# Optimization experiments

Measured on AMD Instinct MI355X. Metric: run time of the kernel, lower is better.

The kernel has to match this reference:

```python
import jax, jax.numpy as jnp
import numpy as np

B, S, IN, OUT = 16, 512, 512, 256
D, H, L, DFF = 1024, 16, 6, 2048
HD = D // H
SCALE = HD ** -0.5
HID = 256  # fc1/fc2 hidden size


def setup_inputs() -> dict:
    key = jax.random.key(0)
    ks = jax.random.split(key, 40)
    g = lambda i, shape, s=0.02: (jax.random.normal(ks[i], shape, jnp.float32) * s)
    z = lambda shape: jnp.zeros(shape, jnp.float32)
    o = lambda shape: jnp.ones(shape, jnp.float32)
    vec = jnp.zeros((B, S), jnp.int32).at[:, 0].set(1)  # one-hot rows (assert-only arg)
    return {
        "x": jax.random.normal(ks[0], (B, S, IN), jnp.float32),
        "xm": jax.random.uniform(ks[1], (B, S), jnp.float32),
        "vecSelector": vec,
        "proj_w": g(2, (IN, D)), "proj_b": z((D,)),
        "pos": g(3, (S, D)),
        "qw": g(4, (L, D, D)), "qb": z((L, D)),
        "kw": g(5, (L, D, D)), "kb": z((L, D)),
        "vw": g(6, (L, D, D)), "vb": z((L, D)),
        "ow": g(7, (L, D, D)), "ob": z((L, D)),
        "ln1_g": o((L, D)), "ln1_b": z((L, D)),
        "ln2_g": o((L, D)), "ln2_b": z((L, D)),
        "w1": g(8, (L, D, DFF)), "b1": z((L, DFF)),
        "w2": g(9, (L, DFF, D)), "b2": z((L, D)),
        "fc1_w": g(10, (D, HID)), "fc1_b": z((HID,)),
        "fc2_w": g(11, (HID, HID)), "fc2_b": z((HID,)),
        "fc3_w": g(12, (HID, OUT)), "fc3_b": z((OUT,)),
    }


def _ln(x, g, b, eps=1e-5):
    m = jnp.mean(x, -1, keepdims=True)
    v = jnp.mean((x - m) ** 2, -1, keepdims=True)
    return (x - m) * jax.lax.rsqrt(v + eps) * g + b


def reference(x, xm, vecSelector, proj_w, proj_b, pos, qw, qb, kw, kb, vw, vb,
              ow, ob, ln1_g, ln1_b, ln2_g, ln2_b, w1, b1, w2, b2,
              fc1_w, fc1_b, fc2_w, fc2_b, fc3_w, fc3_b):
    # linear_proj + positional encoding (pos[:, :d_model] == pos)
    h = x @ proj_w + proj_b + pos  # (B,S,D)
    # key padding mask: whole batch rows masked where xm.sum(-1)==0
    skpm = jnp.broadcast_to((jnp.sum(xm, -1) == 0)[:, None], (B, S))  # (B,S) bool
    neg_inf = jnp.float32(-jnp.inf)
    for i in range(L):
        q = (h @ qw[i] + qb[i]) * SCALE
        k = h @ kw[i] + kb[i]
        v = h @ vw[i] + vb[i]
        q = q.reshape(B, S, H, HD)
        k = k.reshape(B, S, H, HD)
        v = v.reshape(B, S, H, HD)
        sc = jnp.einsum('bthd,bshd->bhts', q, k)  # (B,H,T,S)
        sc = jnp.where(skpm[:, None, None, :], neg_inf, sc)
        # safe_softmax: clamp to [-10,10] THEN softmax (-inf -> -10)
        aw = jax.nn.softmax(jnp.clip(sc, -10.0, 10.0), axis=-1)
        ao = jnp.einsum('bhts,bshd->bthd', aw, v).reshape(B, S, D)
        ao = ao @ ow[i] + ob[i]
        # forward hook: clamp + softmax over embed dim
        ao = jax.nn.softmax(jnp.clip(ao, -10.0, 10.0), axis=-1)
        # torch _sa_block's `[0]` slices batch dim of the raw tensor -> (S,D),
        # broadcast-added to every batch row
        sa = ao[0]
        h = _ln(h + sa[None, :, :], ln1_g[i], ln1_b[i])
        ff = jax.nn.relu(h @ w1[i] + b1[i]) @ w2[i] + b2[i]
        h = _ln(h + ff, ln2_g[i], ln2_b[i])
    out = h @ fc1_w + fc1_b
    for _ in range(5):
        out = out @ fc2_w + fc2_b
    out = out @ fc3_w + fc3_b  # (B,S,OUT)
    return out
```

## Files before the change

### kernel.cpp

```cpp
#include <hip/hip_runtime.h>
#include <hip/hip_bf16.h>

using bf16 = __hip_bfloat16;
typedef __attribute__((ext_vector_type(8))) short short8v;
typedef __attribute__((ext_vector_type(4))) float floatx4;

constexpr int Bc = 16, Sc = 512, INc = 512, OUTc = 256;
constexpr int Dc = 1024, Hc = 16, Lc = 6, DFFc = 2048, HIDc = 256;
constexpr float SCALEc = 0.125f;
constexpr int QKVS = 3072;
constexpr size_t LSLOT = 8388608;

__device__ inline ushort f2b(float f) {
    union { float f; unsigned u; } v; v.f = f;
    unsigned r = (v.u + 0x7FFF + ((v.u >> 16) & 1)) >> 16;
    return (ushort)r;
}
__device__ inline float b2f(ushort b) {
    union { unsigned u; float f; } v; v.u = ((unsigned)b) << 16;
    return v.f;
}
__device__ inline float ldf(const float* p) { return *p; }
__device__ inline float ldf(const ushort* p) { return b2f(*p); }

__device__ inline void gll16(const ushort* g, ushort* l) {
    __builtin_amdgcn_global_load_lds(
        (const __attribute__((address_space(1))) unsigned int*)g,
        (__attribute__((address_space(3))) unsigned int*)l, 16, 0, 0);
}

__device__ inline float blockSum256(float v) {
    __shared__ float tmp[4];
#pragma unroll
    for (int o = 32; o > 0; o >>= 1) v += __shfl_xor(v, o, 64);
    int w = threadIdx.x >> 6;
    __syncthreads();
    if ((threadIdx.x & 63) == 0) tmp[w] = v;
    __syncthreads();
    return tmp[0] + tmp[1] + tmp[2] + tmp[3];
}
__device__ inline float blockMax256(float v) {
    __shared__ float tmp[4];
#pragma unroll
    for (int o = 32; o > 0; o >>= 1) v = fmaxf(v, __shfl_xor(v, o, 64));
    int w = threadIdx.x >> 6;
    __syncthreads();
    if ((threadIdx.x & 63) == 0) tmp[w] = v;
    __syncthreads();
    return fmaxf(fmaxf(tmp[0], tmp[1]), fmaxf(tmp[2], tmp[3]));
}

__global__ __launch_bounds__(256) void mask_k(const float* __restrict__ xm, float* __restrict__ flag) {
    float s = xm[threadIdx.x] + xm[threadIdx.x + 256];
    s = blockSum256(s);
    if (threadIdx.x == 0) flag[0] = (s == 0.f) ? 1.f : 0.f;
}

__global__ __launch_bounds__(256) void cvtx_k(const float* __restrict__ x, ushort* __restrict__ xb) {
    const size_t i = ((size_t)blockIdx.x * 256 + threadIdx.x) * 16;
    __align__(16) ushort o[16];
#pragma unroll
    for (int u = 0; u < 4; ++u) {
        float4 v = *(const float4*)&x[i + u * 4];
        o[u * 4 + 0] = f2b(v.x); o[u * 4 + 1] = f2b(v.y);
        o[u * 4 + 2] = f2b(v.z); o[u * 4 + 3] = f2b(v.w);
    }
    *(short8v*)&xb[i] = *(short8v*)&o[0];
    *(short8v*)&xb[i + 8] = *(short8v*)&o[8];
}

__global__ __launch_bounds__(256) void transp_k(const float* __restrict__ W, ushort* __restrict__ Wt,
                                                int K, int N, float wscale) {
    __shared__ float Ls[64][65];
    const int t = threadIdx.x;
    const int n0 = blockIdx.x * 64, k0 = blockIdx.y * 64;
    const int kr = t >> 4, n4 = (t & 15) * 4;
#pragma unroll
    for (int p = 0; p < 4; ++p) {
        float4 v = *(const float4*)&W[(size_t)(k0 + kr + p * 16) * N + n0 + n4];
        Ls[kr + p * 16][n4 + 0] = v.x; Ls[kr + p * 16][n4 + 1] = v.y;
        Ls[kr + p * 16][n4 + 2] = v.z; Ls[kr + p * 16][n4 + 3] = v.w;
    }
    __syncthreads();
    const int nr = t >> 4, k4 = (t & 15) * 4;
#pragma unroll
    for (int p = 0; p < 4; ++p) {
        ushort4 o;
        o.x = f2b(Ls[k4 + 0][nr + p * 16] * wscale); o.y = f2b(Ls[k4 + 1][nr + p * 16] * wscale);
        o.z = f2b(Ls[k4 + 2][nr + p * 16] * wscale); o.w = f2b(Ls[k4 + 3][nr + p * 16] * wscale);
        *(ushort4*)&Wt[(size_t)(n0 + nr + p * 16) * K + k0 + k4] = o;
    }
}

__global__ __launch_bounds__(256) void transpall_k(
    const float* __restrict__ qw, const float* __restrict__ kw, const float* __restrict__ vw,
    const float* __restrict__ ow, const float* __restrict__ w1, const float* __restrict__ w2,
    ushort* __restrict__ Wt, int l0, size_t lstride)
{
    const int l = l0 + blockIdx.y;
    ushort* slot = Wt + (size_t)blockIdx.y * lstride;
    const int id = blockIdx.x;
    int m, tx, ty;
    if (id < 1024)      { m = id >> 8; int r = id & 255;  tx = r & 15; ty = r >> 4; }
    else if (id < 1536) { m = 4;       int r = id - 1024; tx = r & 31; ty = r >> 5; }
    else                { m = 5;       int r = id - 1536; tx = r & 15; ty = r >> 4; }
    const float* W; ushort* dst; int K, N; float wscale = 1.f;
    switch (m) {
        case 0: W = qw + (size_t)l * Dc * Dc; K = Dc; N = Dc; dst = slot; wscale = SCALEc; break;
        case 1: W = kw + (size_t)l * Dc * Dc; K = Dc; N = Dc; dst = slot + 1048576; break;
        case 2: W = vw + (size_t)l * Dc * Dc; K = Dc; N = Dc; dst = slot + 2097152; break;
        case 3: W = ow + (size_t)l * Dc * Dc; K = Dc; N = Dc; dst = slot + 3145728; break;
        case 4: W = w1 + (size_t)l * Dc * DFFc; K = Dc; N = DFFc; dst = slot + 4194304; break;
        default: W = w2 + (size_t)l * DFFc * Dc; K = DFFc; N = Dc; dst = slot + 6291456; break;
    }
    __shared__ float Ls[64][65];
    const int t = threadIdx.x;
    const int n0 = tx * 64, k0 = ty * 64;
    const int kr = t >> 4, n4 = (t & 15) * 4;
#pragma unroll
    for (int p = 0; p < 4; ++p) {
        float4 v = *(const float4*)&W[(size_t)(k0 + kr + p * 16) * N + n0 + n4];
        Ls[kr + p * 16][n4 + 0] = v.x; Ls[kr + p * 16][n4 + 1] = v.y;
        Ls[kr + p * 16][n4 + 2] = v.z; Ls[kr + p * 16][n4 + 3] = v.w;
    }
    __syncthreads();
#pragma unroll
    for (int p = 0; p < 2; ++p) {
        const int idx = t + 256 * p;
        const int n = idx >> 3, kc = (idx & 7) * 8;
        __align__(16) ushort tmp[8];
#pragma unroll
        for (int u = 0; u < 8; ++u) tmp[u] = f2b(Ls[kc + u][n] * wscale);
        *(short8v*)&dst[(size_t)(n0 + n) * K + k0 + kc] = *(short8v*)tmp;
    }
}

template <int ACT, bool ADDPOS, int OMODE>
__global__ __launch_bounds__(256) void mgemm_k(
    const ushort* __restrict__ A, const ushort* __restrict__ Bt,
    const float* __restrict__ bias, const float* __restrict__ pos,
    float* __restrict__ Cf, ushort* __restrict__ Cb,
    int M, int N, int K, float scale)
{
    __shared__ __align__(16) ushort As[128 * 64];
    __shared__ __align__(16) ushort Bs[128 * 64];
    const int tid = threadIdx.x;
    const int nx = gridDim.x;
    const int nwg = nx * gridDim.y;
    int d = blockIdx.x + blockIdx.y * nx;
    if ((nwg & 7) == 0) d = (d & 7) * (nwg >> 3) + (d >> 3);
    const int m0 = (d / nx) * 128, n0 = (d % nx) * 128;
    const int lane = tid & 63, wv = tid >> 6;
    const int wm = (wv >> 1) * 64, wn = (wv & 1) * 64;
    floatx4 acc[4][4] = {};

    const int rA8 = lane >> 3, cch = lane & 7;

    for (int k0 = 0; k0 < K; k0 += 64) {
#pragma unroll
        for (int p = 0; p < 4; ++p) {
            const int r = wv * 32 + p * 8 + rA8;
            const int cs = (cch ^ (r & 7)) * 8;
            gll16(&Bt[(size_t)(n0 + r) * K + k0 + cs], &Bs[(wv * 32 + p * 8) * 64]);
            gll16(&A[(size_t)(m0 + r) * K + k0 + cs], &As[(wv * 32 + p * 8) * 64]);
        }
        __syncthreads();
#pragma unroll
        for (int s = 0; s < 2; ++s) {
            short8v af[4], bf_[4];
            const int kg = s * 32 + (lane >> 4) * 8;
#pragma unroll
            for (int f = 0; f < 4; ++f) {
                const int ra = wm + f * 16 + (lane & 15);
                af[f] = *(const short8v*)&As[ra * 64 + (kg ^ ((ra & 7) * 8))];
                const int rb = wn + f * 16 + (lane & 15);
                bf_[f] = *(const short8v*)&Bs[rb * 64 + (kg ^ ((rb & 7) * 8))];
            }
#pragma unroll
            for (int i = 0; i < 4; ++i)
#pragma unroll
                for (int j = 0; j < 4; ++j)
                    acc[i][j] = __builtin_amdgcn_mfma_f32_16x16x32_bf16(af[i], bf_[j], acc[i][j], 0, 0, 0);
        }
        __syncthreads();
    }

    const int cc = lane & 15, rr4 = (lane >> 4) * 4;
#pragma unroll
    for (int i = 0; i < 4; ++i) {
#pragma unroll
        for (int j = 0; j < 4; ++j) {
            const int col = n0 + wn + j * 16 + cc;
            const float bsv = bias[col];
#pragma unroll
            for (int q = 0; q < 4; ++q) {
                const int row = m0 + wm + i * 16 + rr4 + q;
                float v = acc[i][j][q] + bsv;
                if (ADDPOS) v += pos[(size_t)(row & (Sc - 1)) * N + col];
                v *= scale;
                if (ACT == 1) v = fmaxf(v, 0.f);
                if (OMODE == 0) Cf[(size_t)row * N + col] = v;
                else if (OMODE == 1) Cb[(size_t)row * N + col] = f2b(v);
                else { Cf[(size_t)row * N + col] = v; Cb[(size_t)row * N + col] = f2b(v); }
            }
        }
    }
}

template <int OMODE>
__global__ __launch_bounds__(256) void mgemm64_k(
    const ushort* __restrict__ A, const ushort* __restrict__ Bt,
    const float* __restrict__ bias,
    float* __restrict__ Cf, ushort* __restrict__ Cb,
    int M, int N, int K)
{
    __shared__ __align__(16) ushort As[64 * 64];
    __shared__ __align__(16) ushort Bs[64 * 64];
    const int tid = threadIdx.x;
    const int nx = gridDim.x;
    const int nwg = nx * gridDim.y;
    int d = blockIdx.x + blockIdx.y * nx;
    if ((nwg & 7) == 0) d = (d & 7) * (nwg >> 3) + (d >> 3);
    const int m0 = (d / nx) * 64, n0 = (d % nx) * 64;
    const int lane = tid & 63, wv = tid >> 6;
    floatx4 acc[4] = {};

    const int rA8 = lane >> 3, cch = lane & 7;

    for (int k0 = 0; k0 < K; k0 += 64) {
#pragma unroll
        for (int p = 0; p < 2; ++p) {
            const int r = wv * 16 + p * 8 + rA8;
            const int cs = (cch ^ (r & 7)) * 8;
            gll16(&A[(size_t)(m0 + r) * K + k0 + cs], &As[(wv * 16 + p * 8) * 64]);
            gll16(&Bt[(size_t)(n0 + r) * K + k0 + cs], &Bs[(wv * 16 + p * 8) * 64]);
        }
        __syncthreads();
#pragma unroll
        for (int s = 0; s < 2; ++s) {
            const int kg = s * 32 + (lane >> 4) * 8;
            const int rb = wv * 16 + (lane & 15);
            short8v bf_ = *(const short8v*)&Bs[rb * 64 + (kg ^ ((rb & 7) * 8))];
#pragma unroll
            for (int f = 0; f < 4; ++f) {
                const int ra = f * 16 + (lane & 15);
                short8v af = *(const short8v*)&As[ra * 64 + (kg ^ ((ra & 7) * 8))];
                acc[f] = __builtin_amdgcn_mfma_f32_16x16x32_bf16(af, bf_, acc[f], 0, 0, 0);
            }
        }
        __syncthreads();
    }

    const int cc = lane & 15, rr4 = (lane >> 4) * 4;
    const int col = n0 + wv * 16 + cc;
    const float bsv = bias[col];
#pragma unroll
    for (int f = 0; f < 4; ++f) {
#pragma unroll
        for (int q = 0; q < 4; ++q) {
            const int row = m0 + f * 16 + rr4 + q;
            float v = acc[f][q] + bsv;
            if (OMODE == 0) Cf[(size_t)row * N + col] = v;
            else            Cb[(size_t)row * N + col] = f2b(v);
        }
    }
}

#define SG256(ts, g) do { \
    if ((ts) < NT) { \
        const int sb_ = (ts) & 1; \
        const int kk_ = (ts) << 6; \
        _Pragma("unroll") \
        for (int ii_ = 0; ii_ < 2; ++ii_) { \
            const int ib_ = wv * 16 + ii_ * 8; \
            if ((g) == 0 || (g) == 2) { \
                const int r0_ = (ib_ < 64 ? ib_ : ib_ + 64) + (((g) == 2) ? 64 : 0); \
                const int rr_ = r0_ + rA8; \
                gll16(A + (size_t)(m0 + rr_) * K + kk_ + ((cch ^ (rr_ & 7)) << 3), \
                      &Al[sb_][r0_ * 64]); \
            } else { \
                const int r0_ = ((ib_ >> 5) * 64) + (ib_ & 31) + (((g) == 3) ? 32 : 0); \
                const int rr_ = r0_ + rA8; \
                gll16(Bt + (size_t)(n0 + rr_) * K + kk_ + ((cch ^ (rr_ & 7)) << 3), \
                      &Bl[sb_][r0_ * 64]); \
            } \
        } \
    } } while (0)

#define LDA256(bb, fb) \
    _Pragma("unroll") for (int f_ = 0; f_ < 4; ++f_) { \
        const int ra_ = wm + ((fb) + f_) * 16 + (lane & 15); \
        const int sw_ = (ra_ & 7) * 8; \
        af[f_][0] = *(const short8v*)&Al[bb][ra_ * 64 + ((kgl) ^ sw_)]; \
        af[f_][1] = *(const short8v*)&Al[bb][ra_ * 64 + ((32 + kgl) ^ sw_)]; }

#define LDB256(bb, jb) \
    _Pragma("unroll") for (int f_ = 0; f_ < 2; ++f_) { \
        const int rb_ = wn + ((jb) + f_) * 16 + (lane & 15); \
        const int sw_ = (rb_ & 7) * 8; \
        bf_[(jb) + f_][0] = *(const short8v*)&Bl[bb][rb_ * 64 + ((kgl) ^ sw_)]; \
        bf_[(jb) + f_][1] = *(const short8v*)&Bl[bb][rb_ * 64 + ((32 + kgl) ^ sw_)]; }

#define MM256(ib, jb) \
    __builtin_amdgcn_s_setprio(1); \
    _Pragma("unroll") for (int i_ = 0; i_ < 4; ++i_) \
    _Pragma("unroll") for (int j_ = 0; j_ < 2; ++j_) \
    _Pragma("unroll") for (int s_ = 0; s_ < 2; ++s_) \
        acc[(ib) + i_][(jb) + j_] = __builtin_amdgcn_mfma_f32_16x16x32_bf16( \
            af[i_][s_], bf_[(jb) + j_][s_], acc[(ib) + i_][(jb) + j_], 0, 0, 0); \
    __builtin_amdgcn_s_setprio(0);

__global__ __launch_bounds__(512) void mgemm256_k(
    const ushort* __restrict__ A, const ushort* __restrict__ Bt,
    const float* __restrict__ bias, ushort* __restrict__ Cb,
    int M, int N, int K, int ACT)
{
    __shared__ __align__(16) ushort Al[2][256 * 64];
    __shared__ __align__(16) ushort Bl[2][256 * 64];
    const int tid = threadIdx.x;
    const int lane = tid & 63, wv = tid >> 6;
    const int nx = gridDim.x, nwg = nx * gridDim.y;
    int d = blockIdx.x + blockIdx.y * nx;
    if ((nwg & 7) == 0) d = (d & 7) * (nwg >> 3) + (d >> 3);
    const int m0 = (d / nx) * 256, n0 = (d % nx) * 256;
    const int wm = (wv >> 2) * 128, wn = (wv & 3) * 64;
    const int rA8 = lane >> 3, cch = lane & 7;
    const int kgl = (lane >> 4) * 8;
    const int NT = K >> 6;
    floatx4 acc[8][4] = {};
    short8v af[4][2], bf_[4][2];

    SG256(0, 0); SG256(0, 1); SG256(0, 2); SG256(0, 3);
    SG256(1, 0); SG256(1, 1); SG256(1, 2);
    asm volatile("s_waitcnt vmcnt(6)" ::: "memory");
    __builtin_amdgcn_s_barrier();

    for (int t = 0; t < NT; ++t) {
        const int bb = t & 1;
        if (t + 1 < NT) { asm volatile("s_waitcnt vmcnt(6)" ::: "memory"); }
        else            { asm volatile("s_waitcnt vmcnt(0)" ::: "memory"); }
        LDA256(bb, 0); LDB256(bb, 0);
        SG256(t + 1, 3);
        __builtin_amdgcn_s_barrier();
        MM256(0, 0);
        __builtin_amdgcn_s_barrier();
        LDB256(bb, 2);
        SG256(t + 2, 0);
        __builtin_amdgcn_s_barrier();
        MM256(0, 2);
        __builtin_amdgcn_s_barrier();
        LDA256(bb, 4);
        SG256(t + 2, 1);
        __builtin_amdgcn_s_barrier();
        MM256(4, 0);
        __builtin_amdgcn_s_barrier();
        SG256(t + 2, 2);
        __builtin_amdgcn_s_barrier();
        MM256(4, 2);
        __builtin_amdgcn_s_barrier();
    }

    const int cc = lane & 15, rr4 = (lane >> 4) * 4;
#pragma unroll
    for (int i = 0; i < 8; ++i) {
#pragma unroll
        for (int j = 0; j < 4; ++j) {
            const int col = n0 + wn + j * 16 + cc;
            const float bsv = bias[col];
#pragma unroll
            for (int q = 0; q < 4; ++q) {
                const int row = m0 + wm + i * 16 + rr4 + q;
                float v = acc[i][j][q] + bsv;
                if (ACT) v = fmaxf(v, 0.f);
                Cb[(size_t)row * N + col] = f2b(v);
            }
        }
    }
}

__global__ __launch_bounds__(256) void fattn_k(
    const ushort* __restrict__ qkv, ushort* __restrict__ ao, const float* __restrict__ flag)
{
    const int hh = blockIdx.y;
    const int t0 = blockIdx.x * 16;
    __shared__ __align__(16) ushort Qs[16 * 64];
    __shared__ __align__(16) ushort Ks[64 * 64];
    __shared__ float Vs[64][68];
    __shared__ float Ps[16][68];
    __shared__ float rs[4][16];
    const int tid = threadIdx.x;
    const int lane = tid & 63, wv = tid >> 6;
    const bool msk = flag[0] > 0.5f;

    if (tid < 128) {
        const int r = tid >> 3, c = tid & 7;
        short8v q = *(const short8v*)&qkv[(size_t)(t0 + r) * QKVS + hh * 64 + c * 8];
        *(short8v*)&Qs[r * 64 + ((c * 8) ^ ((r & 7) * 8))] = q;
    }
    if (tid < 64) ((float*)rs)[tid] = 0.f;

    float o[4] = {};
    const int pq = tid >> 4, pd = (tid & 15) * 4;

    for (int s0 = 0; s0 < Sc; s0 += 64) {
        __syncthreads();
        {
            const int vr = tid >> 2, vc = (tid & 3) * 16;
            const ushort* vsrc = &qkv[(size_t)(s0 + vr) * QKVS + 2048 + hh * 64 + vc];
            short8v v0 = *(const short8v*)vsrc, v1 = *(const short8v*)(vsrc + 8);
#pragma unroll
            for (int u = 0; u < 8; ++u) {
                Vs[vr][vc + u] = b2f((ushort)v0[u]);
                Vs[vr][vc + 8 + u] = b2f((ushort)v1[u]);
            }
#pragma unroll
            for (int u = 0; u < 2; ++u) {
                const int task = tid + u * 256;
                const int kr = task >> 3, kc = task & 7;
                short8v kvv = *(const short8v*)&qkv[(size_t)(s0 + kr) * QKVS + 1024 + hh * 64 + kc * 8];
                *(short8v*)&Ks[kr * 64 + ((kc * 8) ^ ((kr & 7) * 8))] = kvv;
            }
        }
        __syncthreads();
        floatx4 pacc = {};
#pragma unroll
        for (int s = 0; s < 2; ++s) {
            const int kg = s * 32 + (lane >> 4) * 8;
            const int ra = lane & 15;
            short8v aq = *(const short8v*)&Qs[ra * 64 + (kg ^ ((ra & 7) * 8))];
            const int rb = 16 * wv + (lane & 15);
            short8v bk = *(const short8v*)&Ks[rb * 64 + (kg ^ ((rb & 7) * 8))];
            pacc = __builtin_amdgcn_mfma_f32_16x16x32_bf16(aq, bk, pacc, 0, 0, 0);
        }
        const int cc = lane & 15, rr4 = (lane >> 4) * 4;
#pragma unroll
        for (int q = 0; q < 4; ++q) {
            float v = fminf(fmaxf(pacc[q], -10.f), 10.f);
            if (msk) v = -10.f;
            float e = __expf(v - 10.f);
            Ps[rr4 + q][wv * 16 + cc] = e;
            float rsum = e;
            rsum += __shfl_xor(rsum, 1, 64);
            rsum += __shfl_xor(rsum, 2, 64);
            rsum += __shfl_xor(rsum, 4, 64);
            rsum += __shfl_xor(rsum, 8, 64);
            if (cc == 0) rs[wv][rr4 + q] += rsum;
        }
        __syncthreads();
#pragma unroll 8
        for (int ss = 0; ss < 64; ++ss) {
            float p = Ps[pq][ss];
#pragma unroll
            for (int u = 0; u < 4; ++u) o[u] += p * Vs[ss][pd + u];
        }
    }
    __syncthreads();
    float inv = 1.f / (rs[0][pq] + rs[1][pq] + rs[2][pq] + rs[3][pq]);
#pragma unroll
    for (int u = 0; u < 4; ++u)
        ao[(size_t)(t0 + pq) * Dc + hh * 64 + pd + u] = f2b(o[u] * inv);
}

template <int ACT, bool OUT_BF16, bool HASB>
__global__ __launch_bounds__(256) void gemm_k(
    const float* __restrict__ A, const float* __restrict__ W,
    const float* __restrict__ bias,
    float* __restrict__ Cf, bf16* __restrict__ Cb,
    int M, int N, int K, float scale)
{
    __shared__ float As[16][68];
    __shared__ float Ws[16][68];
    const int tid = threadIdx.x;
    const int m0 = blockIdx.y * 64, n0 = blockIdx.x * 64;
    const int ty = tid >> 4, tx = tid & 15;
    float c[4][4] = {};

    const int ka = tid & 15, mb = tid >> 4;
    const int nw = tid & 63, kb = tid >> 6;

    for (int k0 = 0; k0 < K; k0 += 16) {
#pragma unroll
        for (int j = 0; j < 4; ++j) {
            int m = mb + 16 * j;
            As[ka][m] = A[(size_t)(m0 + m) * K + k0 + ka];
        }
#pragma unroll
        for (int j = 0; j < 4; ++j) {
            int k = kb + 4 * j;
            Ws[k][nw] = W[(size_t)(k0 + k) * N + n0 + nw];
        }
        __syncthreads();
#pragma unroll
        for (int k = 0; k < 16; ++k) {
            float4 av = *(const float4*)&As[k][ty * 4];
            float4 wv = *(const float4*)&Ws[k][tx * 4];
            float a[4] = {av.x, av.y, av.z, av.w};
            float w[4] = {wv.x, wv.y, wv.z, wv.w};
#pragma unroll
            for (int i = 0; i < 4; ++i)
#pragma unroll
                for (int j = 0; j < 4; ++j) c[i][j] += a[i] * w[j];
        }
        __syncthreads();
    }

#pragma unroll
    for (int i = 0; i < 4; ++i) {
        int m = m0 + ty * 4 + i;
#pragma unroll
        for (int j = 0; j < 4; ++j) {
            int n = n0 + tx * 4 + j;
            float v = c[i][j] + (HASB ? bias[n] : 0.f);
            v *= scale;
            if (ACT == 1) v = fmaxf(v, 0.f);
            if (OUT_BF16) Cb[(size_t)m * N + n] = __float2bfloat16(v);
            else          Cf[(size_t)m * N + n] = v;
        }
    }
}

__global__ __launch_bounds__(256) void biaschain_k(
    const float* __restrict__ fc1b, const float* __restrict__ fc2w, const float* __restrict__ fc2b,
    const float* __restrict__ fc3w, const float* __restrict__ fc3b, float* __restrict__ bc)
{
    __shared__ float vs[256];
    const int t = threadIdx.x;
    float v = fc1b[t];
    for (int r = 0; r < 5; ++r) {
        vs[t] = v; __syncthreads();
        float s = fc2b[t];
#pragma unroll 8
        for (int k = 0; k < 256; ++k) s += vs[k] * fc2w[k * 256 + t];
        v = s; __syncthreads();
    }
    vs[t] = v; __syncthreads();
    float s = fc3b[t];
#pragma unroll 8
    for (int k = 0; k < 256; ++k) s += vs[k] * fc3w[k * 256 + t];
    bc[t] = s;
}

__global__ __launch_bounds__(256) void qkvbiasall_k(
    const float* __restrict__ qb, const float* __restrict__ kb, const float* __restrict__ vb,
    float* __restrict__ o)
{
    int i = blockIdx.x * 256 + threadIdx.x;
    int l = i / QKVS, j = i - l * QKVS;
    float v = (j < 1024) ? qb[l * Dc + j] * SCALEc
            : (j < 2048) ? kb[l * Dc + j - 1024] : vb[l * Dc + j - 2048];
    o[i] = v;
}

__global__ __launch_bounds__(256) void smaddln_k(
    ushort* __restrict__ hb, const float* __restrict__ obv,
    const float* __restrict__ g, const float* __restrict__ b)
{
    const int row = blockIdx.x;
    const float* op = obv + (size_t)(row & (Sc - 1)) * Dc;
    ushort* hp = hb + (size_t)row * Dc;
    const int c0 = threadIdx.x * 4;
    float4 ov = *(const float4*)&op[c0];
    float r[4] = {ov.x, ov.y, ov.z, ov.w};
    float mx = -1e30f;
#pragma unroll
    for (int j = 0; j < 4; ++j) { r[j] = fminf(fmaxf(r[j], -10.f), 10.f); mx = fmaxf(mx, r[j]); }
    mx = blockMax256(mx);
    float s = 0.f;
#pragma unroll
    for (int j = 0; j < 4; ++j) { r[j] = __expf(r[j] - mx); s += r[j]; }
    s = blockSum256(s);
    float sinv = 1.f / s;
    ushort4 hv = *(const ushort4*)&hp[c0];
    float x[4] = {b2f(hv.x), b2f(hv.y), b2f(hv.z), b2f(hv.w)};
    float ssum = 0.f;
#pragma unroll
    for (int j = 0; j < 4; ++j) { x[j] += r[j] * sinv; ssum += x[j]; }
    float mean = blockSum256(ssum) * (1.f / (float)Dc);
    float vsum = 0.f;
#pragma unroll
    for (int j = 0; j < 4; ++j) { float d_ = x[j] - mean; vsum += d_ * d_; }
    float var = blockSum256(vsum) * (1.f / (float)Dc);
    float inv = rsqrtf(var + 1e-5f);
    float4 gv = *(const float4*)&g[c0];
    float4 bv = *(const float4*)&b[c0];
    ushort4 o4;
    o4.x = f2b((x[0] - mean) * inv * gv.x + bv.x);
    o4.y = f2b((x[1] - mean) * inv * gv.y + bv.y);
    o4.z = f2b((x[2] - mean) * inv * gv.z + bv.z);
    o4.w = f2b((x[3] - mean) * inv * gv.w + bv.w);
    *(ushort4*)&hp[c0] = o4;
}

__global__ __launch_bounds__(256) void add_ln_k(
    ushort* __restrict__ hb, const ushort* __restrict__ add,
    const float* __restrict__ g, const float* __restrict__ b)
{
    const int row = blockIdx.x;
    const ushort* ap = add + (size_t)row * Dc;
    ushort* hp = hb + (size_t)row * Dc;
    const int c0 = threadIdx.x * 4;
    ushort4 hv = *(const ushort4*)&hp[c0];
    float x[4] = {b2f(hv.x), b2f(hv.y), b2f(hv.z), b2f(hv.w)};
#pragma unroll
    for (int j = 0; j < 4; ++j) x[j] += ldf(&ap[c0 + j]);
    float s = x[0] + x[1] + x[2] + x[3];
    float mean = blockSum256(s) * (1.f / (float)Dc);
    float vsum = 0.f;
#pragma unroll
    for (int j = 0; j < 4; ++j) { float d = x[j] - mean; vsum += d * d; }
    float var = blockSum256(vsum) * (1.f / (float)Dc);
    float inv = rsqrtf(var + 1e-5f);
    float4 gv = *(const float4*)&g[c0];
    float4 bv = *(const float4*)&b[c0];
    ushort4 ov;
    ov.x = f2b((x[0] - mean) * inv * gv.x + bv.x);
    ov.y = f2b((x[1] - mean) * inv * gv.y + bv.y);
    ov.z = f2b((x[2] - mean) * inv * gv.z + bv.z);
    ov.w = f2b((x[3] - mean) * inv * gv.w + bv.w);
    *(ushort4*)&hp[c0] = ov;
}

extern "C" void kernel_launch(void* const* d_in, const int* in_sizes, int n_in,
                              void* d_out, int out_size, void* d_ws, size_t ws_size,
                              hipStream_t stream)
{
    const float* x      = (const float*)d_in[0];
    const float* xm     = (const float*)d_in[1];
    const float* proj_w = (const float*)d_in[3];
    const float* proj_b = (const float*)d_in[4];
    const float* pos    = (const float*)d_in[5];
    const float* qw     = (const float*)d_in[6];
    const float* qb     = (const float*)d_in[7];
    const float* kw     = (const float*)d_in[8];
    const float* kb     = (const float*)d_in[9];
    const float* vw     = (const float*)d_in[10];
    const float* vb     = (const float*)d_in[11];
    const float* ow     = (const float*)d_in[12];
    const float* obias  = (const float*)d_in[13];
    const float* ln1g   = (const float*)d_in[14];
    const float* ln1b   = (const float*)d_in[15];
    const float* ln2g   = (const float*)d_in[16];
    const float* ln2b   = (const float*)d_in[17];
    const float* w1     = (const float*)d_in[18];
    const float* b1     = (const float*)d_in[19];
    const float* w2     = (const float*)d_in[20];
    const float* b2     = (const float*)d_in[21];
    const float* fc1w   = (const float*)d_in[22];
    const float* fc1b   = (const float*)d_in[23];
    const float* fc2w   = (const float*)d_in[24];
    const float* fc2b   = (const float*)d_in[25];
    const float* fc3w   = (const float*)d_in[26];
    const float* fc3b   = (const float*)d_in[27];

    float* ws = (float*)d_ws;
    const size_t HSZ = (size_t)Bc * Sc * Dc;
    ushort* hb  = (ushort*)ws;
    ushort* ffu = (ushort*)(ws + HSZ / 2);
    float*  rgA = ws + HSZ;
    float*  meta = ws + 2 * HSZ;
    float*  flag = meta;
    float*  qkvball = meta + 256;
    ushort* Wt = (ushort*)(ws + 2 * HSZ + 262144);

    const bool big = ws_size >= (size_t)163 * 1024 * 1024;
    const size_t lstride = big ? LSLOT : 0;
    ushort* projWt = big ? Wt + (size_t)6 * LSLOT : Wt;

    ushort* qkvfu = (ushort*)rgA;
    ushort* aovu  = (ushort*)(rgA + 786432);
    float*  obv   = rgA + 1048576;
    ushort* midu  = (ushort*)rgA;
    ushort* xb    = (ushort*)rgA;
    float* W2  = rgA;
    float* W4  = rgA + 65536;
    float* W5  = rgA + 131072;
    float* C1  = rgA + 196608;
    float* Wc  = rgA + 458752;
    float* bcv = rgA + 720896;

    const int MR = Bc * Sc;

    mask_k<<<1, 256, 0, stream>>>(xm, flag);
    qkvbiasall_k<<<72, 256, 0, stream>>>(qb, kb, vb, qkvball);
    if (big)
        transpall_k<<<dim3(2048, 6), 256, 0, stream>>>(qw, kw, vw, ow, w1, w2, Wt, 0, lstride);

    cvtx_k<<<(MR * INc) / (256 * 16), 256, 0, stream>>>(x, xb);
    transp_k<<<dim3(Dc / 64, INc / 64), 256, 0, stream>>>(proj_w, projWt, INc, Dc, 1.f);
    mgemm_k<0, true, 1><<<dim3(Dc / 128, MR / 128), 256, 0, stream>>>(
        xb, projWt, proj_b, pos, nullptr, hb, MR, Dc, INc, 1.f);

    for (int l = 0; l < Lc; ++l) {
        ushort* slot = Wt + (size_t)(big ? l : 0) * LSLOT;
        const float* ob_l = obias + l * Dc;
        const float* b1_l = b1 + l * DFFc;
        const float* b2_l = b2 + l * Dc;

        if (!big)
            transpall_k<<<dim3(2048, 1), 256, 0, stream>>>(qw, kw, vw, ow, w1, w2, Wt, l, 0);

        mgemm64_k<1><<<dim3(QKVS / 64, Sc / 64), 256, 0, stream>>>(
            hb, slot, qkvball + l * QKVS, nullptr, qkvfu, Sc, QKVS, Dc);
        fattn_k<<<dim3(Sc / 16, Hc), 256, 0, stream>>>(qkvfu, aovu, flag);
        mgemm64_k<0><<<dim3(Dc / 64, Sc / 64), 256, 0, stream>>>(
            aovu, slot + 3145728, ob_l, obv, nullptr, Sc, Dc, Dc);
        smaddln_k<<<MR, 256, 0, stream>>>(hb, obv, ln1g + l * Dc, ln1b + l * Dc);

        mgemm256_k<<<dim3(DFFc / 256, MR / 256), 512, 0, stream>>>(
            hb, slot + 4194304, b1_l, midu, MR, DFFc, Dc, 1);
        mgemm_k<0, false, 1><<<dim3(Dc / 128, MR / 128), 256, 0, stream>>>(
            midu, slot + 6291456, b2_l, nullptr, nullptr, ffu, MR, Dc, DFFc, 1.f);
        add_ln_k<<<MR, 256, 0, stream>>>(hb, ffu, ln2g + l * Dc, ln2b + l * Dc);
    }

    gemm_k<0, false, false><<<dim3(4, 4), 256, 0, stream>>>(
        fc2w, fc2w, nullptr, W2, nullptr, HIDc, HIDc, HIDc, 1.f);
    gemm_k<0, false, false><<<dim3(4, 4), 256, 0, stream>>>(
        W2, W2, nullptr, W4, nullptr, HIDc, HIDc, HIDc, 1.f);
    gemm_k<0, false, false><<<dim3(4, 4), 256, 0, stream>>>(
        W4, fc2w, nullptr, W5, nullptr, HIDc, HIDc, HIDc, 1.f);
    gemm_k<0, false, false><<<dim3(4, 16), 256, 0, stream>>>(
        fc1w, W5, nullptr, C1, nullptr, Dc, HIDc, HIDc, 1.f);
    gemm_k<0, false, false><<<dim3(4, 16), 256, 0, stream>>>(
        C1, fc3w, nullptr, Wc, nullptr, Dc, HIDc, HIDc, 1.f);
    biaschain_k<<<1, 256, 0, stream>>>(fc1b, fc2w, fc2b, fc3w, fc3b, bcv);
    transp_k<<<dim3(HIDc / 64, Dc / 64), 256, 0, stream>>>(Wc, Wt, Dc, HIDc, 1.f);
    mgemm64_k<0><<<dim3(HIDc / 64, MR / 64), 256, 0, stream>>>(
        hb, Wt, bcv, (float*)d_out, nullptr, MR, HIDc, Dc);
}
```

Before: 1.215 ms.

## Add 256x128 pipelined MFMA GEMM for w2 and projection; enlarge transpose tiles

Adds a new 512-thread GEMM kernel with 256x128 tiles, double-buffered LDS and direct global-to-LDS loads. It replaces the 128x128 kernel for the FFN w2 GEMM and the input projection, aiming for more operand reuse per workgroup and better overlap of loads with MFMA work. The 256x256 kernel's vmcnt wait is moved to the end of each iteration so loads stay in flight across the MFMA phases. The weight transpose kernel now handles 256x64 tiles per block, launching a quarter as many blocks, at the cost of a larger LDS footprint.

```diff
diff --git a/kernel.cpp b/kernel.cpp
--- a/kernel.cpp
+++ b/kernel.cpp
@@ -101,9 +101,9 @@
     ushort* slot = Wt + (size_t)blockIdx.y * lstride;
     const int id = blockIdx.x;
     int m, tx, ty;
-    if (id < 1024)      { m = id >> 8; int r = id & 255;  tx = r & 15; ty = r >> 4; }
-    else if (id < 1536) { m = 4;       int r = id - 1024; tx = r & 31; ty = r >> 5; }
-    else                { m = 5;       int r = id - 1536; tx = r & 15; ty = r >> 4; }
+    if (id < 256)      { m = id >> 6; int r = id & 63;  tx = r & 15; ty = r >> 4; }
+    else if (id < 384) { m = 4;       int r = id - 256; tx = r & 31; ty = r >> 5; }
+    else               { m = 5;       int r = id - 384; tx = r & 15; ty = r >> 4; }
     const float* W; ushort* dst; int K, N; float wscale = 1.f;
     switch (m) {
         case 0: W = qw + (size_t)l * Dc * Dc; K = Dc; N = Dc; dst = slot; wscale = SCALEc; break;
@@ -113,21 +113,22 @@
         case 4: W = w1 + (size_t)l * Dc * DFFc; K = Dc; N = DFFc; dst = slot + 4194304; break;
         default: W = w2 + (size_t)l * DFFc * Dc; K = DFFc; N = Dc; dst = slot + 6291456; break;
     }
-    __shared__ float Ls[64][65];
+    __shared__ float Ls[256][65];
     const int t = threadIdx.x;
-    const int n0 = tx * 64, k0 = ty * 64;
-    const int kr = t >> 4, n4 = (t & 15) * 4;
-#pragma unroll
-    for (int p = 0; p < 4; ++p) {
-        float4 v = *(const float4*)&W[(size_t)(k0 + kr + p * 16) * N + n0 + n4];
-        Ls[kr + p * 16][n4 + 0] = v.x; Ls[kr + p * 16][n4 + 1] = v.y;
-        Ls[kr + p * 16][n4 + 2] = v.z; Ls[kr + p * 16][n4 + 3] = v.w;
+    const int n0 = tx * 64, k0 = ty * 256;
+    const int krb = t >> 4, n4 = (t & 15) * 4;
+#pragma unroll
+    for (int p = 0; p < 16; ++p) {
+        const int r = krb + p * 16;
+        float4 v = *(const float4*)&W[(size_t)(k0 + r) * N + n0 + n4];
+        Ls[r][n4 + 0] = v.x; Ls[r][n4 + 1] = v.y;
+        Ls[r][n4 + 2] = v.z; Ls[r][n4 + 3] = v.w;
     }
     __syncthreads();
 #pragma unroll
-    for (int p = 0; p < 2; ++p) {
+    for (int p = 0; p < 8; ++p) {
         const int idx = t + 256 * p;
-        const int n = idx >> 3, kc = (idx & 7) * 8;
+        const int n = idx >> 5, kc = (idx & 31) * 8;
         __align__(16) ushort tmp[8];
 #pragma unroll
         for (int u = 0; u < 8; ++u) tmp[u] = f2b(Ls[kc + u][n] * wscale);
@@ -337,8 +338,6 @@
 
     for (int t = 0; t < NT; ++t) {
         const int bb = t & 1;
-        if (t + 1 < NT) { asm volatile("s_waitcnt vmcnt(6)" ::: "memory"); }
-        else            { asm volatile("s_waitcnt vmcnt(0)" ::: "memory"); }
         LDA256(bb, 0); LDB256(bb, 0);
         SG256(t + 1, 3);
         __builtin_amdgcn_s_barrier();
@@ -357,6 +356,8 @@
         SG256(t + 2, 2);
         __builtin_amdgcn_s_barrier();
         MM256(4, 2);
+        if (t + 2 < NT) { asm volatile("s_waitcnt vmcnt(6)" ::: "memory"); }
+        else            { asm volatile("s_waitcnt vmcnt(0)" ::: "memory"); }
         __builtin_amdgcn_s_barrier();
     }
 
@@ -376,6 +377,126 @@
             }
         }
     }
+}
+
+__global__ __launch_bounds__(512) void mgemm256x128_k(
+    const ushort* __restrict__ A, const ushort* __restrict__ Bt,
+    const float* __restrict__ bias, const float* __restrict__ pos, int addpos,
+    float* __restrict__ Cf, ushort* __restrict__ Cb, int omode,
+    int M, int N, int K, int ACT)
+{
+    __shared__ __align__(16) ushort Al[2][256 * 64];
+    __shared__ __align__(16) ushort Bl[2][128 * 64];
+    const int tid = threadIdx.x;
+    const int lane = tid & 63, wv = tid >> 6;
+    const int nx = gridDim.x, nwg = nx * gridDim.y;
+    int d = blockIdx.x + blockIdx.y * nx;
+    if ((nwg & 7) == 0) d = (d & 7) * (nwg >> 3) + (d >> 3);
+    const int m0 = (d / nx) * 256, n0 = (d % nx) * 128;
+    const int wm = (wv >> 1) * 64, wn = (wv & 1) * 64;
+    const int rA8 = lane >> 3, cch = lane & 7;
+    const int kgl = (lane >> 4) * 8;
+    const int NT = K >> 6;
+    floatx4 acc[4][4] = {};
+    short8v af[2][2], bf_[4][2];
+
+#define SGA(ts, g) do { \
+    if ((ts) < NT) { \
+        const int sb_ = (ts) & 1; \
+        const int kk_ = (ts) << 6; \
+        _Pragma("unroll") \
+        for (int ii_ = 0; ii_ < 2; ++ii_) { \
+            const int r0_ = (wv >> 1) * 64 + ((g) ? 32 : 0) + (wv & 1) * 16 + ii_ * 8; \
+            const int rr_ = r0_ + rA8; \
+            gll16(A + (size_t)(m0 + rr_) * K + kk_ + ((cch ^ (rr_ & 7)) << 3), \
+                  &Al[sb_][r0_ * 64]); \
+        } \
+    } } while (0)
+#define SGB(ts) do { \
+    if ((ts) < NT) { \
+        const int sb_ = (ts) & 1; \
+        const int kk_ = (ts) << 6; \
+        _Pragma("unroll") \
+        for (int ii_ = 0; ii_ < 2; ++ii_) { \
+            const int r0_ = wv * 16 + ii_ * 8; \
+            const int rr_ = r0_ + rA8; \
+            gll16(Bt + (size_t)(n0 + rr_) * K + kk_ + ((cch ^ (rr_ & 7)) << 3), \
+                  &Bl[sb_][r0_ * 64]); \
+        } \
+    } } while (0)
+#define LDAX(bb, fb) \
+    _Pragma("unroll") for (int f_ = 0; f_ < 2; ++f_) { \
+        const int ra_ = wm + ((fb) + f_) * 16 + (lane & 15); \
+        const int sw_ = (ra_ & 7) * 8; \
+        af[f_][0] = *(const short8v*)&Al[bb][ra_ * 64 + ((kgl) ^ sw_)]; \
+        af[f_][1] = *(const short8v*)&Al[bb][ra_ * 64 + ((32 + kgl) ^ sw_)]; }
+#define LDBX(bb, jb) \
+    _Pragma("unroll") for (int f_ = 0; f_ < 2; ++f_) { \
+        const int rb_ = wn + ((jb) + f_) * 16 + (lane & 15); \
+        const int sw_ = (rb_ & 7) * 8; \
+        bf_[(jb) + f_][0] = *(const short8v*)&Bl[bb][rb_ * 64 + ((kgl) ^ sw_)]; \
+        bf_[(jb) + f_][1] = *(const short8v*)&Bl[bb][rb_ * 64 + ((32 + kgl) ^ sw_)]; }
+#define MMX(ia, jb) \
+    __builtin_amdgcn_s_setprio(1); \
+    _Pragma("unroll") for (int i_ = 0; i_ < 2; ++i_) \
+    _Pragma("unroll") for (int j_ = 0; j_ < 2; ++j_) \
+    _Pragma("unroll") for (int s_ = 0; s_ < 2; ++s_) \
+        acc[(ia) + i_][(jb) + j_] = __builtin_amdgcn_mfma_f32_16x16x32_bf16( \
+            af[i_][s_], bf_[(jb) + j_][s_], acc[(ia) + i_][(jb) + j_], 0, 0, 0); \
+    __builtin_amdgcn_s_setprio(0);
+
+    SGA(0, 0); SGA(0, 1); SGB(0);
+    SGA(1, 0); SGA(1, 1);
+    asm volatile("s_waitcnt vmcnt(4)" ::: "memory");
+    __builtin_amdgcn_s_barrier();
+
+    for (int t = 0; t < NT; ++t) {
+        const int bb = t & 1;
+        LDAX(bb, 0); LDBX(bb, 0);
+        SGB(t + 1);
+        __builtin_amdgcn_s_barrier();
+        MMX(0, 0);
+        __builtin_amdgcn_s_barrier();
+        LDBX(bb, 2);
+        SGA(t + 2, 0);
+        __builtin_amdgcn_s_barrier();
+        MMX(0, 2);
+        __builtin_amdgcn_s_barrier();
+        LDAX(bb, 2);
+        __builtin_amdgcn_s_barrier();
+        MMX(2, 0);
+        __builtin_amdgcn_s_barrier();
+        SGA(t + 2, 1);
+        __builtin_amdgcn_s_barrier();
+        MMX(2, 2);
+        if (t + 2 < NT) { asm volatile("s_waitcnt vmcnt(4)" ::: "memory"); }
+        else            { asm volatile("s_waitcnt vmcnt(0)" ::: "memory"); }
+        __builtin_amdgcn_s_barrier();
+    }
+
+    const int cc = lane & 15, rr4 = (lane >> 4) * 4;
+#pragma unroll
+    for (int i = 0; i < 4; ++i) {
+#pragma unroll
+        for (int j = 0; j < 4; ++j) {
+            const int col = n0 + wn + j * 16 + cc;
+            const float bsv = bias[col];
+#pragma unroll
+            for (int q = 0; q < 4; ++q) {
+                const int row = m0 + wm + i * 16 + rr4 + q;
+                float v = acc[i][j][q] + bsv;
+                if (addpos) v += pos[(size_t)(row & (Sc - 1)) * N + col];
+                if (ACT) v = fmaxf(v, 0.f);
+                if (omode == 0) Cf[(size_t)row * N + col] = v;
+                else            Cb[(size_t)row * N + col] = f2b(v);
+            }
+        }
+    }
+#undef SGA
+#undef SGB
+#undef LDAX
+#undef LDBX
+#undef MMX
 }
 
 __global__ __launch_bounds__(256) void fattn_k(
@@ -683,12 +804,12 @@
     mask_k<<<1, 256, 0, stream>>>(xm, flag);
     qkvbiasall_k<<<72, 256, 0, stream>>>(qb, kb, vb, qkvball);
     if (big)
-        transpall_k<<<dim3(2048, 6), 256, 0, stream>>>(qw, kw, vw, ow, w1, w2, Wt, 0, lstride);
+        transpall_k<<<dim3(512, 6), 256, 0, stream>>>(qw, kw, vw, ow, w1, w2, Wt, 0, lstride);
 
     cvtx_k<<<(MR * INc) / (256 * 16), 256, 0, stream>>>(x, xb);
     transp_k<<<dim3(Dc / 64, INc / 64), 256, 0, stream>>>(proj_w, projWt, INc, Dc, 1.f);
-    mgemm_k<0, true, 1><<<dim3(Dc / 128, MR / 128), 256, 0, stream>>>(
-        xb, projWt, proj_b, pos, nullptr, hb, MR, Dc, INc, 1.f);
+    mgemm256x128_k<<<dim3(Dc / 128, MR / 256), 512, 0, stream>>>(
+        xb, projWt, proj_b, pos, 1, nullptr, hb, 1, MR, Dc, INc, 0);
 
     for (int l = 0; l < Lc; ++l) {
         ushort* slot = Wt + (size_t)(big ? l : 0) * LSLOT;
@@ -697,7 +818,7 @@
         const float* b2_l = b2 + l * Dc;
 
         if (!big)
-            transpall_k<<<dim3(2048, 1), 256, 0, stream>>>(qw, kw, vw, ow, w1, w2, Wt, l, 0);
+            transpall_k<<<dim3(512, 1), 256, 0, stream>>>(qw, kw, vw, ow, w1, w2, Wt, l, 0);
 
         mgemm64_k<1><<<dim3(QKVS / 64, Sc / 64), 256, 0, stream>>>(
             hb, slot, qkvball + l * QKVS, nullptr, qkvfu, Sc, QKVS, Dc);
@@ -708,8 +829,8 @@
 
         mgemm256_k<<<dim3(DFFc / 256, MR / 256), 512, 0, stream>>>(
             hb, slot + 4194304, b1_l, midu, MR, DFFc, Dc, 1);
-        mgemm_k<0, false, 1><<<dim3(Dc / 128, MR / 128), 256, 0, stream>>>(
-            midu, slot + 6291456, b2_l, nullptr, nullptr, ffu, MR, Dc, DFFc, 1.f);
+        mgemm256x128_k<<<dim3(Dc / 128, MR / 256), 512, 0, stream>>>(
+            midu, slot + 6291456, b2_l, nullptr, 0, nullptr, ffu, 1, MR, Dc, DFFc, 0);
         add_ln_k<<<MR, 256, 0, stream>>>(hb, ffu, ln2g + l * Dc, ln2b + l * Dc);
     }
 
```

Measured after the change: 1.282 ms. 5.5% more time.
